# Optimization experiments

Hardware: AMD Instinct MI355X
Metric: run time of the kernel (lower is better)

Reference implementation:

```python
import jax, jax.numpy as jnp
import numpy as np

B, T, D = 2, 2048, 1024
H, DK, DV, M = 4, 256, 256, 256  # heads, head_k_dim, head_v_dim, num_slots
GATE_NORM = 8.0
SCALE = 1.0
EPS = 1e-5


def setup_inputs() -> dict:
    key = jax.random.key(0)
    ks = jax.random.split(key, 7)
    w = lambda k, shp: jax.random.normal(k, shp, dtype=jnp.float32) * 0.02
    return {
        "hidden_states": jax.random.normal(ks[0], (B, T, D), dtype=jnp.float32),
        "Wq": w(ks[1], (H * DK, D)),   # q_proj
        "Wk": w(ks[2], (H * DK, D)),   # k_proj (num_kv_groups == 1)
        "Wv": w(ks[3], (H * DV, D)),   # v_proj
        "Wf": w(ks[4], (H * M, D)),    # f_proj (num_kv_heads * num_slots)
        "g_w": jnp.ones((H * DV,), dtype=jnp.float32),  # RMSNorm weight
        "Wo": w(ks[5], (D, H * DV)),   # o_proj
    }


def _gsa(q, k, v, s, f, scale):
    """Two-pass GLA recurrence (GSA). All inputs time-major [T,B,H,*]."""
    Bb, Hh = q.shape[1], q.shape[2]
    gk = jnp.exp(f)  # [T,B,H,M] decay in (0,1)

    # Pass 1: Hk_t = Hk_{t-1} * g_t (over slot dim) + k_t (x) s_t ; ok_t = q_t @ Hk_t
    def step1(S, inp):
        qt, kt, st, gt = inp
        S = S * gt[..., None, :] + kt[..., :, None] * st[..., None, :]
        return S, jnp.einsum('bhk,bhkm->bhm', qt * scale, S)

    S0k = jnp.zeros((Bb, Hh, DK, M), q.dtype)
    _, ok = jax.lax.scan(step1, S0k, (q, k, s, gk))

    qv = jax.nn.softmax(ok, axis=-1)  # [T,B,H,M]

    # Pass 2: Hv_t = Hv_{t-1} * g_t (over slot dim) + s_t (x) v_t ; o_t = qv_t @ Hv_t
    def step2(S, inp):
        qt, st, vt, gt = inp
        S = S * gt[..., :, None] + st[..., :, None] * vt[..., None, :]
        return S, jnp.einsum('bhm,bhmv->bhv', qt, S)

    S0v = jnp.zeros((Bb, Hh, M, DV), q.dtype)
    _, ov = jax.lax.scan(step2, S0v, (qv, s, v, gk))
    return ov  # [T,B,H,DV]


def reference(hidden_states, Wq, Wk, Wv, Wf, g_w, Wo):
    Bb, Tt, Dd = hidden_states.shape
    q = (hidden_states @ Wq.T).reshape(Bb, Tt, H, DK)
    k = (hidden_states @ Wk.T).reshape(Bb, Tt, H, DK)
    v = (hidden_states @ Wv.T).reshape(Bb, Tt, H, DV)
    f = (hidden_states @ Wf.T).reshape(Bb, Tt, H, M)

    q = jax.nn.silu(q)            # swish feature map
    k = jax.nn.silu(k)
    v = jax.nn.silu(v)
    f = jax.nn.log_sigmoid(f) / GATE_NORM   # forget-gate log decay
    s = 1.0 - jnp.exp(f)                     # slot write strength

    tm = lambda x: jnp.transpose(x, (1, 0, 2, 3))  # -> time-major
    ov = _gsa(tm(q), tm(k), tm(v), tm(s), tm(f), SCALE)
    o = jnp.transpose(ov, (1, 0, 2, 3)).reshape(Bb, Tt, H * DV)

    # rms_norm_linear(silu(o), g_norm.weight, None, Wo, None), norm in fp32
    o = jax.nn.silu(o)
    o32 = o.astype(jnp.float32)
    rms = o32 * jax.lax.rsqrt(jnp.mean(o32 * o32, axis=-1, keepdims=True) + EPS)
    return (rms * g_w).astype(hidden_states.dtype) @ Wo.T
```

## Files before the change

kernel.cpp:

```cpp
#include <hip/hip_runtime.h>
#include <math.h>

#define TLEN 2048
#define NROWS 4096
#define CHK 64
#define NCHK 32

typedef unsigned short u16;
typedef unsigned int u32;
typedef __attribute__((ext_vector_type(8))) short bf16x8;
typedef __attribute__((ext_vector_type(4))) float f32x4;

#define MFMA(a, b, c) __builtin_amdgcn_mfma_f32_16x16x32_bf16(a, b, c, 0, 0, 0)

__device__ __forceinline__ float bf2f(u16 u) {
    u32 v = ((u32)u) << 16; float f; __builtin_memcpy(&f, &v, 4); return f;
}
__device__ __forceinline__ u16 f2bf(float x) {
    u32 u; __builtin_memcpy(&u, &x, 4);
    u += 0x7FFFu + ((u >> 16) & 1u);
    return (u16)(u >> 16);
}
__device__ __forceinline__ u32 pack2bf(float a, float b) {
    return (u32)f2bf(a) | ((u32)f2bf(b) << 16);
}
__device__ __forceinline__ float bflo(u32 u) { return bf2f((u16)(u & 0xFFFFu)); }
__device__ __forceinline__ float bfhi(u32 u) { return bf2f((u16)(u >> 16)); }
__device__ __forceinline__ float siluf(float x) { return x / (1.f + expf(-x)); }

__global__ void gsa_detect(const u32* __restrict__ gw, int* __restrict__ flag) {
    *flag = (gw[0] == 0x3F803F80u) ? 1 : 0;
}

__global__ __launch_bounds__(256) void gsa_tobf16(const void* __restrict__ src,
        u16* __restrict__ dst, int n8, const int* __restrict__ flag) {
    int i = blockIdx.x * 256 + threadIdx.x;
    if (i >= n8) return;
    if (*flag) {
        ((uint4*)dst)[i] = ((const uint4*)src)[i];
    } else {
        float4 a = ((const float4*)src)[2 * i];
        float4 b = ((const float4*)src)[2 * i + 1];
        uint4 o;
        o.x = pack2bf(a.x, a.y); o.y = pack2bf(a.z, a.w);
        o.z = pack2bf(b.x, b.y); o.w = pack2bf(b.z, b.w);
        ((uint4*)dst)[i] = o;
    }
}

__global__ __launch_bounds__(256) void gsa_emit(const float* __restrict__ src,
        void* __restrict__ dst, int n4, const int* __restrict__ flag) {
    int i = blockIdx.x * 256 + threadIdx.x;
    if (i >= n4) return;
    float4 v = ((const float4*)src)[i];
    if (*flag) {
        uint2 u; u.x = pack2bf(v.x, v.y); u.y = pack2bf(v.z, v.w);
        ((uint2*)dst)[i] = u;
    } else {
        ((float4*)dst)[i] = v;
    }
}

__global__ __launch_bounds__(256) void gsa_gemm_direct(const u16* __restrict__ A,
        const u16* __restrict__ W0, const u16* __restrict__ W1,
        const u16* __restrict__ W2, const u16* __restrict__ W3,
        void* __restrict__ O0, void* __restrict__ O1,
        void* __restrict__ O2, void* __restrict__ O3, int actpack, int obfmask) {
    int tid = threadIdx.x;
    int sel = blockIdx.x >> 3;
    int ntile = blockIdx.x & 7;
    int mtile = blockIdx.y;
    const u16* W = (sel == 0) ? W0 : (sel == 1) ? W1 : (sel == 2) ? W2 : W3;
    void* Out    = (sel == 0) ? O0 : (sel == 1) ? O1 : (sel == 2) ? O2 : O3;
    int act = (actpack >> (sel * 8)) & 0xff;
    int obf = (obfmask >> sel) & 1;
    int w = tid >> 6, lane = tid & 63;
    int wm = w >> 1, wn = w & 1;
    int frow = lane & 15, fq = lane >> 4;
    const u16* Ap[4];
    const u16* Bp[4];
    #pragma unroll
    for (int i = 0; i < 4; i++) {
        Ap[i] = A + (size_t)(mtile * 128 + wm * 64 + i * 16 + frow) * 1024 + fq * 8;
        Bp[i] = W + (size_t)(ntile * 128 + wn * 64 + i * 16 + frow) * 1024 + fq * 8;
    }
    f32x4 acc[4][4];
    #pragma unroll
    for (int i = 0; i < 4; i++)
        #pragma unroll
        for (int j = 0; j < 4; j++) acc[i][j] = (f32x4){0.f, 0.f, 0.f, 0.f};

    bf16x8 afA[4], bfA[4], afB[4], bfB[4];
    #pragma unroll
    for (int i = 0; i < 4; i++) {
        afA[i] = *(const bf16x8*)(Ap[i]);
        bfA[i] = *(const bf16x8*)(Bp[i]);
    }
    for (int k0 = 0; k0 < 1024; k0 += 64) {
        #pragma unroll
        for (int i = 0; i < 4; i++) {
            afB[i] = *(const bf16x8*)(Ap[i] + k0 + 32);
            bfB[i] = *(const bf16x8*)(Bp[i] + k0 + 32);
        }
        #pragma unroll
        for (int mt = 0; mt < 4; mt++)
            #pragma unroll
            for (int nt = 0; nt < 4; nt++)
                acc[mt][nt] = MFMA(afA[mt], bfA[nt], acc[mt][nt]);
        if (k0 + 64 < 1024) {
            #pragma unroll
            for (int i = 0; i < 4; i++) {
                afA[i] = *(const bf16x8*)(Ap[i] + k0 + 64);
                bfA[i] = *(const bf16x8*)(Bp[i] + k0 + 64);
            }
        }
        #pragma unroll
        for (int mt = 0; mt < 4; mt++)
            #pragma unroll
            for (int nt = 0; nt < 4; nt++)
                acc[mt][nt] = MFMA(afB[mt], bfB[nt], acc[mt][nt]);
    }
    #pragma unroll
    for (int mt = 0; mt < 4; mt++) {
        #pragma unroll
        for (int nt = 0; nt < 4; nt++) {
            #pragma unroll
            for (int r = 0; r < 4; r++) {
                float x = acc[mt][nt][r];
                int grow = mtile * 128 + wm * 64 + mt * 16 + fq * 4 + r;
                int gcol = ntile * 128 + wn * 64 + nt * 16 + frow;
                float val;
                if (act == 0) val = siluf(x);
                else if (act == 1) {
                    float ls = (x >= 0.f) ? -log1pf(expf(-x)) : (x - log1pf(expf(x)));
                    val = expf(0.125f * ls);
                } else val = x;
                size_t o = (size_t)grow * 1024 + gcol;
                if (obf) ((u16*)Out)[o] = f2bf(val);
                else     ((float*)Out)[o] = val;
            }
        }
    }
}

template<int P>
__global__ __launch_bounds__(256) void gsa_p_local(const u16* __restrict__ Xb,
        const float* __restrict__ GKp, u16* __restrict__ Sb, float* __restrict__ ECb) {
    __shared__ u16 Xt[256 * 72];
    __shared__ u16 Wt[256 * 72];
    int tid = threadIdx.x;
    int bh = blockIdx.x & 7, c = blockIdx.x >> 3;
    int b = bh >> 2, h = bh & 3, t0 = c * CHK;
    size_t gbase = ((size_t)(b * TLEN + t0)) * 1024 + h * 256;
    {
        const u16* xp = Xb + gbase + tid;
        #pragma unroll
        for (int t8 = 0; t8 < 8; t8++) {
            bf16x8 v;
            #pragma unroll
            for (int j = 0; j < 8; j++) v[j] = (short)xp[(size_t)(t8 * 8 + j) * 1024];
            *(bf16x8*)&Xt[tid * 72 + t8 * 8] = v;
        }
    }
    {
        float g[CHK], f[CHK];
        const float* gp = GKp + gbase + tid;
        #pragma unroll
        for (int t = 0; t < CHK; t++) g[t] = gp[(size_t)t * 1024];
        float phiC = 0.f;
        #pragma unroll
        for (int t = 0; t < CHK; t++) { f[t] = __logf(g[t]); phiC += f[t]; }
        if (P == 1) ECb[(bh * NCHK + c) * 256 + tid] = __expf(phiC);
        float phi = 0.f;
        #pragma unroll
        for (int t8 = 0; t8 < 8; t8++) {
            bf16x8 v;
            #pragma unroll
            for (int j = 0; j < 8; j++) {
                phi += f[t8 * 8 + j];
                v[j] = (short)f2bf((1.f - g[t8 * 8 + j]) * __expf(phiC - phi));
            }
            *(bf16x8*)&Wt[tid * 72 + t8 * 8] = v;
        }
    }
    __syncthreads();
    int w = tid >> 6, lane = tid & 63, frow = lane & 15, fq = lane >> 4;
    const u16* Arows = (P == 1) ? Wt : Xt;
    const u16* Brows = (P == 1) ? Xt : Wt;
    bf16x8 afr[4][2];
    #pragma unroll
    for (int it = 0; it < 4; it++)
        #pragma unroll
        for (int ks = 0; ks < 2; ks++)
            afr[it][ks] = *(const bf16x8*)&Arows[(w * 64 + it * 16 + frow) * 72 + ks * 32 + fq * 8];
    u16* Sp = Sb + (size_t)(bh * NCHK + c) * 65536;
    for (int jt = 0; jt < 16; jt++) {
        f32x4 ac[4];
        #pragma unroll
        for (int it = 0; it < 4; it++) ac[it] = (f32x4){0.f, 0.f, 0.f, 0.f};
        #pragma unroll
        for (int ks = 0; ks < 2; ks++) {
            bf16x8 bfr = *(const bf16x8*)&Brows[(jt * 16 + frow) * 72 + ks * 32 + fq * 8];
            #pragma unroll
            for (int it = 0; it < 4; it++) ac[it] = MFMA(afr[it][ks], bfr, ac[it]);
        }
        #pragma unroll
        for (int it = 0; it < 4; it++)
            #pragma unroll
            for (int r = 0; r < 4; r++)
                Sp[(size_t)(w * 64 + it * 16 + fq * 4 + r) * 256 + jt * 16 + frow]
                    = f2bf(ac[it][r]);
    }
}

__global__ __launch_bounds__(256) void gsa_scan1(u16* __restrict__ Sb,
        const float* __restrict__ ECb) {
    int bh = blockIdx.x & 7, part = blockIdx.x >> 3;
    int lin = part * 1024 + threadIdx.x * 4;
    int m = lin >> 8, k = lin & 255;
    u16* Sp = Sb + (size_t)bh * NCHK * 65536 + m * 256 + k;
    const float* Ep = ECb + bh * NCHK * 256 + m;
    float s0 = 0.f, s1 = 0.f, s2 = 0.f, s3 = 0.f;
    for (int c = 0; c < NCHK; c++) {
        uint2 d = *(uint2*)(Sp + (size_t)c * 65536);
        float ec = Ep[c * 256];
        uint2 o; o.x = pack2bf(s0, s1); o.y = pack2bf(s2, s3);
        *(uint2*)(Sp + (size_t)c * 65536) = o;
        s0 = fmaf(ec, s0, bflo(d.x)); s1 = fmaf(ec, s1, bfhi(d.x));
        s2 = fmaf(ec, s2, bflo(d.y)); s3 = fmaf(ec, s3, bfhi(d.y));
    }
}
__global__ __launch_bounds__(256) void gsa_scan2(u16* __restrict__ Sb,
        const float* __restrict__ ECb) {
    int bh = blockIdx.x & 7, part = blockIdx.x >> 3;
    int lin = part * 1024 + threadIdx.x * 4;
    int v = lin >> 8, m = lin & 255;
    u16* Sp = Sb + (size_t)bh * NCHK * 65536 + v * 256 + m;
    const float* Ep = ECb + bh * NCHK * 256 + m;
    float s0 = 0.f, s1 = 0.f, s2 = 0.f, s3 = 0.f;
    for (int c = 0; c < NCHK; c++) {
        uint2 d = *(uint2*)(Sp + (size_t)c * 65536);
        float4 e = *(const float4*)(Ep + c * 256);
        uint2 o; o.x = pack2bf(s0, s1); o.y = pack2bf(s2, s3);
        *(uint2*)(Sp + (size_t)c * 65536) = o;
        s0 = fmaf(e.x, s0, bflo(d.x)); s1 = fmaf(e.y, s1, bfhi(d.x));
        s2 = fmaf(e.z, s2, bflo(d.y)); s3 = fmaf(e.w, s3, bfhi(d.y));
    }
}

__global__ __launch_bounds__(256) void gsa_p1_out(const u16* __restrict__ Qb,
        const u16* __restrict__ Kb, const float* __restrict__ GKp,
        const u16* __restrict__ Sb, float* __restrict__ OK) {
    __shared__ u16 Qs[64 * 264];
    __shared__ float Asc[64 * 68];
    __shared__ float Gs[64 * 260];
    int tid = threadIdx.x;
    int bh = blockIdx.x & 7, c = blockIdx.x >> 3;
    int b = bh >> 2, h = bh & 3, t0 = c * CHK;
    size_t gbase = ((size_t)(b * TLEN + t0)) * 1024 + h * 256;
    #pragma unroll
    for (int j = 0; j < 8; j++) {
        int lin = j * 256 + tid;
        int t = lin >> 5, kg = (lin & 31) * 8;
        *(bf16x8*)&Qs[t * 264 + kg] = *(const bf16x8*)(Qb + gbase + (size_t)t * 1024 + kg);
    }
    __syncthreads();
    int w = tid >> 6, lane = tid & 63, frow = lane & 15, fq = lane >> 4;
    {
        const u16* Kg = Kb + gbase;
        #pragma unroll
        for (int tt = 0; tt < 4; tt++) {
            f32x4 ac = (f32x4){0.f, 0.f, 0.f, 0.f};
            #pragma unroll
            for (int ks = 0; ks < 8; ks++) {
                bf16x8 a = *(const bf16x8*)&Qs[(w * 16 + frow) * 264 + ks * 32 + fq * 8];
                bf16x8 bb = *(const bf16x8*)(Kg + (size_t)(tt * 16 + frow) * 1024 + ks * 32 + fq * 8);
                ac = MFMA(a, bb, ac);
            }
            #pragma unroll
            for (int r = 0; r < 4; r++) {
                int t = w * 16 + fq * 4 + r, tau = tt * 16 + frow;
                Asc[t * 68 + tau] = (tau <= t) ? ac[r] : 0.f;
            }
        }
    }
    {
        const u16* Sg = Sb + (size_t)(bh * NCHK + c) * 65536;
        f32x4 gac[4][4];
        #pragma unroll
        for (int tt = 0; tt < 4; tt++)
            #pragma unroll
            for (int mt = 0; mt < 4; mt++) gac[tt][mt] = (f32x4){0.f, 0.f, 0.f, 0.f};
        for (int ks = 0; ks < 8; ks++) {
            bf16x8 bfr[4], afr[4];
            #pragma unroll
            for (int mt = 0; mt < 4; mt++)
                bfr[mt] = *(const bf16x8*)(Sg + (size_t)(w * 64 + mt * 16 + frow) * 256 + ks * 32 + fq * 8);
            #pragma unroll
            for (int tt = 0; tt < 4; tt++)
                afr[tt] = *(const bf16x8*)&Qs[(tt * 16 + frow) * 264 + ks * 32 + fq * 8];
            #pragma unroll
            for (int tt = 0; tt < 4; tt++)
                #pragma unroll
                for (int mt = 0; mt < 4; mt++)
                    gac[tt][mt] = MFMA(afr[tt], bfr[mt], gac[tt][mt]);
        }
        #pragma unroll
        for (int tt = 0; tt < 4; tt++)
            #pragma unroll
            for (int mt = 0; mt < 4; mt++)
                #pragma unroll
                for (int r = 0; r < 4; r++)
                    Gs[(tt * 16 + fq * 4 + r) * 260 + w * 64 + mt * 16 + frow] = gac[tt][mt][r];
    }
    __syncthreads();
    float E[CHK], U[CHK];
    {
        float g[CHK];
        const float* gp = GKp + gbase + tid;
        #pragma unroll
        for (int t = 0; t < CHK; t++) g[t] = gp[(size_t)t * 1024];
        float phi = 0.f;
        #pragma unroll
        for (int t = 0; t < CHK; t++) {
            float f = __logf(g[t]); phi += f;
            E[t] = __expf(phi);
            U[t] = (1.f - g[t]) * __expf(-phi);
        }
    }
    float* okp = OK + gbase + tid;
    #pragma unroll
    for (int t = 0; t < CHK; t++) {
        float acc = 0.f;
        const int NG = (t < 32) ? 8 : 16;
        #pragma unroll
        for (int j = 0; j < NG; j++) {
            float4 a4 = *(const float4*)&Asc[t * 68 + j * 4];
            acc = fmaf(a4.x, U[4 * j + 0], acc);
            acc = fmaf(a4.y, U[4 * j + 1], acc);
            acc = fmaf(a4.z, U[4 * j + 2], acc);
            acc = fmaf(a4.w, U[4 * j + 3], acc);
        }
        okp[(size_t)t * 1024] = E[t] * (Gs[t * 260 + tid] + acc);
    }
}

__global__ __launch_bounds__(256) void gsa_softmax(float* __restrict__ x) {
    int row = blockIdx.x * 4 + (threadIdx.x >> 6);
    int lane = threadIdx.x & 63;
    float* p = x + (size_t)row * 256 + lane * 4;
    float4 v = *(float4*)p;
    float mx = fmaxf(fmaxf(v.x, v.y), fmaxf(v.z, v.w));
    #pragma unroll
    for (int off = 32; off; off >>= 1) mx = fmaxf(mx, __shfl_xor(mx, off));
    v.x = expf(v.x - mx); v.y = expf(v.y - mx);
    v.z = expf(v.z - mx); v.w = expf(v.w - mx);
    float sm = v.x + v.y + v.z + v.w;
    #pragma unroll
    for (int off = 32; off; off >>= 1) sm += __shfl_xor(sm, off);
    float inv = 1.f / sm;
    v.x *= inv; v.y *= inv; v.z *= inv; v.w *= inv;
    *(float4*)p = v;
}

__global__ __launch_bounds__(256) void gsa_p2_out(const float* __restrict__ QV,
        const u16* __restrict__ Vb, const float* __restrict__ GKp,
        const u16* __restrict__ Sb, float* __restrict__ OV) {
    __shared__ u16 qe[64 * 264];
    __shared__ u16 Us[64 * 264];
    __shared__ float Bsc[64 * 68];
    __shared__ float Gs[64 * 260];
    int tid = threadIdx.x;
    int bh = blockIdx.x & 7, c = blockIdx.x >> 3;
    int b = bh >> 2, h = bh & 3, t0 = c * CHK;
    size_t gbase = ((size_t)(b * TLEN + t0)) * 1024 + h * 256;
    {
        float g[CHK], qv[CHK];
        const float* gp = GKp + gbase + tid;
        const float* qp = QV + gbase + tid;
        #pragma unroll
        for (int t = 0; t < CHK; t++) g[t] = gp[(size_t)t * 1024];
        #pragma unroll
        for (int t = 0; t < CHK; t++) qv[t] = qp[(size_t)t * 1024];
        float phi = 0.f;
        #pragma unroll
        for (int t = 0; t < CHK; t++) {
            float f = __logf(g[t]); phi += f;
            float E = __expf(phi);
            qe[t * 264 + tid] = f2bf(qv[t] * E);
            Us[t * 264 + tid] = f2bf((1.f - g[t]) * __expf(-phi));
        }
    }
    __syncthreads();
    int w = tid >> 6, lane = tid & 63, frow = lane & 15, fq = lane >> 4;
    {
        const u16* Sg = Sb + (size_t)(bh * NCHK + c) * 65536;
        f32x4 gac[4][4];
        #pragma unroll
        for (int tt = 0; tt < 4; tt++)
            #pragma unroll
            for (int vt = 0; vt < 4; vt++) gac[tt][vt] = (f32x4){0.f, 0.f, 0.f, 0.f};
        for (int ks = 0; ks < 8; ks++) {
            bf16x8 bfr[4], afr[4];
            #pragma unroll
            for (int vt = 0; vt < 4; vt++)
                bfr[vt] = *(const bf16x8*)(Sg + (size_t)(w * 64 + vt * 16 + frow) * 256 + ks * 32 + fq * 8);
            #pragma unroll
            for (int tt = 0; tt < 4; tt++)
                afr[tt] = *(const bf16x8*)&qe[(tt * 16 + frow) * 264 + ks * 32 + fq * 8];
            #pragma unroll
            for (int tt = 0; tt < 4; tt++)
                #pragma unroll
                for (int vt = 0; vt < 4; vt++)
                    gac[tt][vt] = MFMA(afr[tt], bfr[vt], gac[tt][vt]);
        }
        #pragma unroll
        for (int tt = 0; tt < 4; tt++)
            #pragma unroll
            for (int vt = 0; vt < 4; vt++)
                #pragma unroll
                for (int r = 0; r < 4; r++)
                    Gs[(tt * 16 + fq * 4 + r) * 260 + w * 64 + vt * 16 + frow] = gac[tt][vt][r];
    }
    {
        #pragma unroll
        for (int tt = 0; tt < 4; tt++) {
            f32x4 ac = (f32x4){0.f, 0.f, 0.f, 0.f};
            #pragma unroll
            for (int ks = 0; ks < 8; ks++) {
                bf16x8 a = *(const bf16x8*)&qe[(w * 16 + frow) * 264 + ks * 32 + fq * 8];
                bf16x8 bb = *(const bf16x8*)&Us[(tt * 16 + frow) * 264 + ks * 32 + fq * 8];
                ac = MFMA(a, bb, ac);
            }
            #pragma unroll
            for (int r = 0; r < 4; r++) {
                int t = w * 16 + fq * 4 + r, tau = tt * 16 + frow;
                Bsc[t * 68 + tau] = (tau <= t) ? ac[r] : 0.f;
            }
        }
    }
    __syncthreads();
    float vcol[CHK];
    {
        const u16* vp = Vb + gbase + tid;
        #pragma unroll
        for (int t = 0; t < CHK; t++) vcol[t] = bf2f(vp[(size_t)t * 1024]);
    }
    float* ovp = OV + gbase + tid;
    #pragma unroll
    for (int t = 0; t < CHK; t++) {
        float acc = 0.f;
        const int NG = (t < 32) ? 8 : 16;
        #pragma unroll
        for (int j = 0; j < NG; j++) {
            float4 a4 = *(const float4*)&Bsc[t * 68 + j * 4];
            acc = fmaf(a4.x, vcol[4 * j + 0], acc);
            acc = fmaf(a4.y, vcol[4 * j + 1], acc);
            acc = fmaf(a4.z, vcol[4 * j + 2], acc);
            acc = fmaf(a4.w, vcol[4 * j + 3], acc);
        }
        ovp[(size_t)t * 1024] = Gs[t * 260 + tid] + acc;
    }
}

__global__ __launch_bounds__(256) void gsa_rmsnorm(const float* __restrict__ ov,
        const void* __restrict__ gw, const int* __restrict__ flag,
        u16* __restrict__ out) {
    __shared__ float part[4];
    int row = blockIdx.x;
    int tid = threadIdx.x;
    const float* p = ov + (size_t)row * 1024 + tid * 4;
    float4 x = *(const float4*)p;
    float y0 = siluf(x.x), y1 = siluf(x.y), y2 = siluf(x.z), y3 = siluf(x.w);
    float ssum = y0 * y0 + y1 * y1 + y2 * y2 + y3 * y3;
    #pragma unroll
    for (int off = 32; off; off >>= 1) ssum += __shfl_xor(ssum, off);
    if ((tid & 63) == 0) part[tid >> 6] = ssum;
    __syncthreads();
    float tot = part[0] + part[1] + part[2] + part[3];
    float r = rsqrtf(tot * (1.f / 1024.f) + 1e-5f);
    float4 g;
    if (*flag) {
        ushort4 u = ((const ushort4*)gw)[tid];
        g.x = bf2f(u.x); g.y = bf2f(u.y); g.z = bf2f(u.z); g.w = bf2f(u.w);
    } else {
        g = ((const float4*)gw)[tid];
    }
    ushort4 o;
    o.x = f2bf(y0 * r * g.x); o.y = f2bf(y1 * r * g.y);
    o.z = f2bf(y2 * r * g.z); o.w = f2bf(y3 * r * g.w);
    ((ushort4*)(out + (size_t)row * 1024))[tid] = o;
}

extern "C" void kernel_launch(void* const* d_in, const int* in_sizes, int n_in,
                              void* d_out, int out_size, void* d_ws, size_t ws_size,
                              hipStream_t stream) {
    (void)in_sizes; (void)n_in; (void)out_size; (void)ws_size;
    const void* hs_raw = d_in[0];
    const void* wq_raw = d_in[1];
    const void* wk_raw = d_in[2];
    const void* wv_raw = d_in[3];
    const void* wf_raw = d_in[4];
    const void* gw_raw = d_in[5];
    const void* wo_raw = d_in[6];

    char* base = (char*)d_ws;
    int* flag = (int*)base;
    float* fb = (float*)(base + 256);
    const size_t F1M = 1048576;
    u16* Qb   = (u16*)fb;
    u16* Kb   = (u16*)(fb + 2 * F1M);
    u16* Vb   = (u16*)(fb + 4 * F1M);
    float* GK = fb + 6 * F1M;
    float* OK = fb + 10 * F1M;
    u16* Sbuf = (u16*)(fb + 14 * F1M);
    float* ECb = fb + 14 * F1M + 8388608;
    u16* Wb   = (u16*)(fb + 14 * F1M + 8388608 + 65536);
    u16* WQb = Wb;
    u16* WKb = Wb + 1048576;
    u16* WVb = Wb + 2 * 1048576;
    u16* WFb = Wb + 3 * 1048576;
    u16* WOb = Wb + 4 * 1048576;
    u16* HSb  = (u16*)OK;
    float* OV = fb;
    u16* AN   = (u16*)OK;
    float* FO = GK;

    gsa_detect<<<1, 1, 0, stream>>>((const u32*)gw_raw, flag);
    gsa_tobf16<<<2048, 256, 0, stream>>>(hs_raw, HSb, 524288, flag);
    gsa_tobf16<<<512, 256, 0, stream>>>(wq_raw, WQb, 131072, flag);
    gsa_tobf16<<<512, 256, 0, stream>>>(wk_raw, WKb, 131072, flag);
    gsa_tobf16<<<512, 256, 0, stream>>>(wv_raw, WVb, 131072, flag);
    gsa_tobf16<<<512, 256, 0, stream>>>(wf_raw, WFb, 131072, flag);
    gsa_tobf16<<<512, 256, 0, stream>>>(wo_raw, WOb, 131072, flag);

    gsa_gemm_direct<<<dim3(32, 32), 256, 0, stream>>>(HSb, WQb, WKb, WVb, WFb,
            Qb, Kb, Vb, GK, 0x01000000, 0x7);

    gsa_p_local<1><<<256, 256, 0, stream>>>(Kb, GK, Sbuf, ECb);
    gsa_scan1<<<512, 256, 0, stream>>>(Sbuf, ECb);
    gsa_p1_out<<<256, 256, 0, stream>>>(Qb, Kb, GK, Sbuf, OK);
    gsa_softmax<<<4096, 256, 0, stream>>>(OK);
    gsa_p_local<2><<<256, 256, 0, stream>>>(Vb, GK, Sbuf, ECb);
    gsa_scan2<<<512, 256, 0, stream>>>(Sbuf, ECb);
    gsa_p2_out<<<256, 256, 0, stream>>>(OK, Vb, GK, Sbuf, OV);

    gsa_rmsnorm<<<4096, 256, 0, stream>>>(OV, gw_raw, flag, AN);
    gsa_gemm_direct<<<dim3(8, 32), 256, 0, stream>>>(AN, WOb, WOb, WOb, WOb,
            FO, FO, FO, FO, 0x02020202, 0x0);
    gsa_emit<<<4096, 256, 0, stream>>>(FO, d_out, 1048576, flag);
}
```

Before: 513.5 us.

## Restructure projection GEMMs into row-stripe blocks with A staged in LDS

After: 928.7 us. 80.9% more time.

```diff
diff --git a/kernel.cpp b/kernel.cpp
--- a/kernel.cpp
+++ b/kernel.cpp
@@ -61,83 +61,105 @@
     }
 }
 
-__global__ __launch_bounds__(256) void gsa_gemm_direct(const u16* __restrict__ A,
+__global__ __launch_bounds__(256, 2) void gsa_gemm_stripe(const u16* __restrict__ A,
         const u16* __restrict__ W0, const u16* __restrict__ W1,
         const u16* __restrict__ W2, const u16* __restrict__ W3,
         void* __restrict__ O0, void* __restrict__ O1,
-        void* __restrict__ O2, void* __restrict__ O3, int actpack, int obfmask) {
+        void* __restrict__ O2, void* __restrict__ O3,
+        int actpack, int obfmask, int selbits) {
+    __shared__ u16 As[32 * 1032];
     int tid = threadIdx.x;
-    int sel = blockIdx.x >> 3;
-    int ntile = blockIdx.x & 7;
-    int mtile = blockIdx.y;
+    int sel = blockIdx.x & ((1 << selbits) - 1);
+    int stripe = blockIdx.x >> selbits;
     const u16* W = (sel == 0) ? W0 : (sel == 1) ? W1 : (sel == 2) ? W2 : W3;
     void* Out    = (sel == 0) ? O0 : (sel == 1) ? O1 : (sel == 2) ? O2 : O3;
     int act = (actpack >> (sel * 8)) & 0xff;
     int obf = (obfmask >> sel) & 1;
-    int w = tid >> 6, lane = tid & 63;
-    int wm = w >> 1, wn = w & 1;
-    int frow = lane & 15, fq = lane >> 4;
-    const u16* Ap[4];
-    const u16* Bp[4];
-    #pragma unroll
-    for (int i = 0; i < 4; i++) {
-        Ap[i] = A + (size_t)(mtile * 128 + wm * 64 + i * 16 + frow) * 1024 + fq * 8;
-        Bp[i] = W + (size_t)(ntile * 128 + wn * 64 + i * 16 + frow) * 1024 + fq * 8;
-    }
-    f32x4 acc[4][4];
-    #pragma unroll
-    for (int i = 0; i < 4; i++)
-        #pragma unroll
-        for (int j = 0; j < 4; j++) acc[i][j] = (f32x4){0.f, 0.f, 0.f, 0.f};
-
-    bf16x8 afA[4], bfA[4], afB[4], bfB[4];
-    #pragma unroll
-    for (int i = 0; i < 4; i++) {
-        afA[i] = *(const bf16x8*)(Ap[i]);
-        bfA[i] = *(const bf16x8*)(Bp[i]);
-    }
-    for (int k0 = 0; k0 < 1024; k0 += 64) {
-        #pragma unroll
-        for (int i = 0; i < 4; i++) {
-            afB[i] = *(const bf16x8*)(Ap[i] + k0 + 32);
-            bfB[i] = *(const bf16x8*)(Bp[i] + k0 + 32);
-        }
-        #pragma unroll
-        for (int mt = 0; mt < 4; mt++)
-            #pragma unroll
-            for (int nt = 0; nt < 4; nt++)
-                acc[mt][nt] = MFMA(afA[mt], bfA[nt], acc[mt][nt]);
-        if (k0 + 64 < 1024) {
-            #pragma unroll
-            for (int i = 0; i < 4; i++) {
-                afA[i] = *(const bf16x8*)(Ap[i] + k0 + 64);
-                bfA[i] = *(const bf16x8*)(Bp[i] + k0 + 64);
-            }
-        }
-        #pragma unroll
-        for (int mt = 0; mt < 4; mt++)
-            #pragma unroll
-            for (int nt = 0; nt < 4; nt++)
-                acc[mt][nt] = MFMA(afB[mt], bfB[nt], acc[mt][nt]);
-    }
-    #pragma unroll
-    for (int mt = 0; mt < 4; mt++) {
-        #pragma unroll
-        for (int nt = 0; nt < 4; nt++) {
-            #pragma unroll
-            for (int r = 0; r < 4; r++) {
-                float x = acc[mt][nt][r];
-                int grow = mtile * 128 + wm * 64 + mt * 16 + fq * 4 + r;
-                int gcol = ntile * 128 + wn * 64 + nt * 16 + frow;
-                float val;
-                if (act == 0) val = siluf(x);
-                else if (act == 1) {
-                    float ls = (x >= 0.f) ? -log1pf(expf(-x)) : (x - log1pf(expf(x)));
-                    val = expf(0.125f * ls);
-                } else val = x;
-                size_t o = (size_t)grow * 1024 + gcol;
-                if (obf) ((u16*)Out)[o] = f2bf(val);
-                else     ((float*)Out)[o] = val;
+    int r0 = stripe * 32;
+    #pragma unroll
+    for (int j = 0; j < 16; j++) {
+        int idx = j * 256 + tid;
+        int row = idx >> 7, c8 = (idx & 127) * 8;
+        *(bf16x8*)&As[row * 1032 + c8] =
+            *(const bf16x8*)(A + (size_t)(r0 + row) * 1024 + c8);
+    }
+    __syncthreads();
+    int w = tid >> 6, lane = tid & 63, frow = lane & 15, fq = lane >> 4;
+    const u16* ap0 = &As[frow * 1032 + fq * 8];
+    const u16* ap1 = &As[(16 + frow) * 1032 + fq * 8];
+    for (int nt = 0; nt < 4; nt++) {
+        const u16* bp[4];
+        #pragma unroll
+        for (int t = 0; t < 4; t++)
+            bp[t] = W + (size_t)(nt * 256 + w * 64 + t * 16 + frow) * 1024 + fq * 8;
+        f32x4 acc[2][4];
+        #pragma unroll
+        for (int mt = 0; mt < 2; mt++)
+            #pragma unroll
+            for (int t = 0; t < 4; t++) acc[mt][t] = (f32x4){0.f, 0.f, 0.f, 0.f};
+        bf16x8 aX[2][2], bX[4][2], aY[2][2], bY[4][2];
+        #pragma unroll
+        for (int s = 0; s < 2; s++) {
+            aX[0][s] = *(const bf16x8*)(ap0 + s * 32);
+            aX[1][s] = *(const bf16x8*)(ap1 + s * 32);
+            #pragma unroll
+            for (int t = 0; t < 4; t++) bX[t][s] = *(const bf16x8*)(bp[t] + s * 32);
+        }
+        for (int kb = 0; kb < 16; kb += 2) {
+            int koY = (kb + 1) * 64;
+            #pragma unroll
+            for (int s = 0; s < 2; s++) {
+                aY[0][s] = *(const bf16x8*)(ap0 + koY + s * 32);
+                aY[1][s] = *(const bf16x8*)(ap1 + koY + s * 32);
+                #pragma unroll
+                for (int t = 0; t < 4; t++)
+                    bY[t][s] = *(const bf16x8*)(bp[t] + koY + s * 32);
+            }
+            #pragma unroll
+            for (int s = 0; s < 2; s++)
+                #pragma unroll
+                for (int mt = 0; mt < 2; mt++)
+                    #pragma unroll
+                    for (int t = 0; t < 4; t++)
+                        acc[mt][t] = MFMA(aX[mt][s], bX[t][s], acc[mt][t]);
+            if (kb + 2 < 16) {
+                int koX = (kb + 2) * 64;
+                #pragma unroll
+                for (int s = 0; s < 2; s++) {
+                    aX[0][s] = *(const bf16x8*)(ap0 + koX + s * 32);
+                    aX[1][s] = *(const bf16x8*)(ap1 + koX + s * 32);
+                    #pragma unroll
+                    for (int t = 0; t < 4; t++)
+                        bX[t][s] = *(const bf16x8*)(bp[t] + koX + s * 32);
+                }
+            }
+            #pragma unroll
+            for (int s = 0; s < 2; s++)
+                #pragma unroll
+                for (int mt = 0; mt < 2; mt++)
+                    #pragma unroll
+                    for (int t = 0; t < 4; t++)
+                        acc[mt][t] = MFMA(aY[mt][s], bY[t][s], acc[mt][t]);
+        }
+        #pragma unroll
+        for (int mt = 0; mt < 2; mt++) {
+            #pragma unroll
+            for (int t = 0; t < 4; t++) {
+                #pragma unroll
+                for (int r = 0; r < 4; r++) {
+                    float x = acc[mt][t][r];
+                    int grow = r0 + mt * 16 + fq * 4 + r;
+                    int gcol = nt * 256 + w * 64 + t * 16 + frow;
+                    float val;
+                    if (act == 0) val = siluf(x);
+                    else if (act == 1) {
+                        float ls = (x >= 0.f) ? -log1pf(expf(-x)) : (x - log1pf(expf(x)));
+                        val = expf(0.125f * ls);
+                    } else val = x;
+                    size_t o = (size_t)grow * 1024 + gcol;
+                    if (obf) ((u16*)Out)[o] = f2bf(val);
+                    else     ((float*)Out)[o] = val;
+                }
             }
         }
     }
@@ -534,8 +556,8 @@
     gsa_tobf16<<<512, 256, 0, stream>>>(wf_raw, WFb, 131072, flag);
     gsa_tobf16<<<512, 256, 0, stream>>>(wo_raw, WOb, 131072, flag);
 
-    gsa_gemm_direct<<<dim3(32, 32), 256, 0, stream>>>(HSb, WQb, WKb, WVb, WFb,
-            Qb, Kb, Vb, GK, 0x01000000, 0x7);
+    gsa_gemm_stripe<<<512, 256, 0, stream>>>(HSb, WQb, WKb, WVb, WFb,
+            Qb, Kb, Vb, GK, 0x01000000, 0x7, 2);
 
     gsa_p_local<1><<<256, 256, 0, stream>>>(Kb, GK, Sbuf, ECb);
     gsa_scan1<<<512, 256, 0, stream>>>(Sbuf, ECb);
@@ -546,7 +568,7 @@
     gsa_p2_out<<<256, 256, 0, stream>>>(OK, Vb, GK, Sbuf, OV);
 
     gsa_rmsnorm<<<4096, 256, 0, stream>>>(OV, gw_raw, flag, AN);
-    gsa_gemm_direct<<<dim3(8, 32), 256, 0, stream>>>(AN, WOb, WOb, WOb, WOb,
-            FO, FO, FO, FO, 0x02020202, 0x0);
+    gsa_gemm_stripe<<<128, 256, 0, stream>>>(AN, WOb, WOb, WOb, WOb,
+            FO, FO, FO, FO, 0x02020202, 0x0, 0);
     gsa_emit<<<4096, 256, 0, stream>>>(FO, d_out, 1048576, flag);
 }
```
